# Optimization experiments

Measured on AMD Instinct MI355X. Metric: run time of the kernel, lower is better.

Reference implementation:

```python
import jax, jax.numpy as jnp
import numpy as np

EPS = 1e-5
K_NBR = 21   # num_neighbors + 1 (self)
PSI = 4


def _bn(x, g, b):
    # BatchNorm (training-mode forward): channel-last, normalize over all other axes
    axes = tuple(range(x.ndim - 1))
    m = jnp.mean(x, axis=axes, keepdims=True)
    v = jnp.var(x, axis=axes, keepdims=True)
    return (x - m) * jax.lax.rsqrt(v + EPS) * g + b


def setup_inputs() -> dict:
    key = jax.random.key(0)
    ks = jax.random.split(key, 16)
    B, N, Cin, Cout = 4, 2048, 64, 256
    h = Cout // 2
    w_ch = Cout // PSI
    heads = 2 * PSI - 1

    def w(k, o, i):
        return jax.random.normal(k, (o, i), dtype=jnp.float32) * (1.0 / np.sqrt(i))

    p = {}
    p['xyz'] = jax.random.normal(ks[0], (B, N, 3), dtype=jnp.float32)
    p['f'] = jax.random.normal(ks[1], (B, Cin, N), dtype=jnp.float32)
    p['W_geo'] = w(ks[2], h, 6);       p['g_geo'] = jnp.ones(h);   p['b_geo'] = jnp.zeros(h)
    p['W_feat'] = w(ks[3], h, 2 * Cin); p['g_feat'] = jnp.ones(h); p['b_feat'] = jnp.zeros(h)
    p['g_bn'] = jnp.ones(Cout); p['b_bn'] = jnp.zeros(Cout)
    p['W_q'] = w(ks[4], Cout, Cout); p['g_q'] = jnp.ones(Cout); p['b_q'] = jnp.zeros(Cout)
    p['W_k'] = w(ks[5], Cout, Cout); p['g_k'] = jnp.ones(Cout); p['b_k'] = jnp.zeros(Cout)
    p['W_v'] = w(ks[6], Cout, Cout); p['g_v'] = jnp.ones(Cout); p['b_v'] = jnp.zeros(Cout)
    p['W_fus'] = w(ks[7], Cout, heads * w_ch); p['bias_fus'] = jnp.zeros(Cout)
    p['g_fus'] = jnp.ones(Cout); p['b_fus'] = jnp.zeros(Cout)
    p['g_ln'] = jnp.ones(Cout); p['b_ln'] = jnp.zeros(Cout)
    p['W_mlp'] = w(ks[8], Cout, Cout); p['bias_mlp'] = jnp.zeros(Cout)
    return p


def reference(xyz, f, W_geo, g_geo, b_geo, W_feat, g_feat, b_feat, g_bn, b_bn,
              W_q, g_q, b_q, W_k, g_k, b_k, W_v, g_v, b_v,
              W_fus, bias_fus, g_fus, b_fus, g_ln, b_ln, W_mlp, bias_mlp):
    B, N, _ = xyz.shape
    Cout = g_bn.shape[0]
    w_ch = Cout // PSI
    d_sh = w_ch // 2
    heads = 2 * PSI - 1

    # ---- PositionFusion: KNN grouping ----
    sq = jnp.sum(xyz * xyz, axis=-1)                                   # [B,N]
    d2 = sq[:, :, None] + sq[:, None, :] - 2.0 * jnp.einsum('bnd,bmd->bnm', xyz, xyz)
    _, idx = jax.lax.top_k(-d2, K_NBR)                                 # [B,N,K]

    grouped_xyz = jax.vmap(lambda p, i: p[i])(xyz, idx)                # [B,N,K,3]
    xyz_diff = grouped_xyz - xyz[:, :, None, :]
    geo_in = jnp.concatenate(
        [jnp.broadcast_to(xyz[:, :, None, :], grouped_xyz.shape), xyz_diff], axis=-1)  # [B,N,K,6]

    ft = jnp.transpose(f, (0, 2, 1))                                   # [B,N,Cin]
    grouped_f = jax.vmap(lambda p, i: p[i])(ft, idx)                   # [B,N,K,Cin]
    feat_in = jnp.concatenate(
        [grouped_f, jnp.broadcast_to(ft[:, :, None, :], grouped_f.shape)], axis=-1)    # [B,N,K,2Cin]

    geo = jax.nn.relu(_bn(jnp.einsum('bnki,oi->bnko', geo_in, W_geo), g_geo, b_geo))
    fea = jax.nn.relu(_bn(jnp.einsum('bnki,oi->bnko', feat_in, W_feat), g_feat, b_feat))
    feature_ = jnp.max(jnp.concatenate([geo, fea], axis=-1), axis=2)   # [B,N,Cout] (maxpool over K)

    # ---- BatchNorm1d ----
    x = _bn(feature_, g_bn, b_bn)

    # ---- Shifted-channel multi-head attention ----
    q = jax.nn.relu(_bn(jnp.einsum('bnc,oc->bno', x, W_q), g_q, b_q))
    k = jax.nn.relu(_bn(jnp.einsum('bnc,oc->bno', x, W_k), g_k, b_k))
    v = jax.nn.relu(_bn(jnp.einsum('bnc,oc->bno', x, W_v), g_v, b_v))

    qh = jnp.stack([q[..., m * d_sh:m * d_sh + w_ch] for m in range(heads)], axis=1)  # [B,H,N,w]
    kh = jnp.stack([k[..., m * d_sh:m * d_sh + w_ch] for m in range(heads)], axis=1)
    vh = jnp.stack([v[..., m * d_sh:m * d_sh + w_ch] for m in range(heads)], axis=1)

    a = jax.nn.softmax(jnp.einsum('bhnc,bhmc->bhnm', qh, kh), axis=-1)  # [B,H,N,N]
    o = jnp.einsum('bhnm,bhmc->bhnc', a, vh)                            # [B,H,N,w]
    O = jnp.transpose(o, (0, 2, 1, 3)).reshape(B, N, heads * w_ch)      # channel-concat per head

    fus = jax.nn.relu(_bn(jnp.einsum('bnc,oc->bno', O, W_fus) + bias_fus, g_fus, b_fus))

    feature__ = fus + feature_                                          # residual

    # ---- LayerNorm over channels ----
    m = jnp.mean(feature__, axis=-1, keepdims=True)
    var = jnp.var(feature__, axis=-1, keepdims=True)
    y = (feature__ - m) * jax.lax.rsqrt(var + EPS) * g_ln + b_ln

    out = feature__ + (jnp.einsum('bnc,oc->bno', y, W_mlp) + bias_mlp)
    return jnp.transpose(out, (0, 2, 1))                                # [B,Cout,N] like torch
```

## Files before the change

### kernel.cpp

```cpp
#include <hip/hip_runtime.h>
#include <math.h>

#define NB    4
#define NPTS  2048
#define ROWS  (NB*NPTS)
#define CIN   64
#define COUT  256
#define KNBR  21
#define NHEADS 7
#define WCH   64
#define DSH   32
#define LOG2E 1.4426950408889634f

typedef __attribute__((ext_vector_type(8))) short short8;
typedef __attribute__((ext_vector_type(4))) float floatx4;

#if __has_builtin(__builtin_amdgcn_exp2f)
#define EXP2(x) __builtin_amdgcn_exp2f(x)
#else
#define EXP2(x) __expf((x)*0.6931471805599453f)
#endif
#if __has_builtin(__builtin_amdgcn_rcpf)
#define RCP(x) __builtin_amdgcn_rcpf(x)
#else
#define RCP(x) (1.0f/(x))
#endif

__device__ __forceinline__ ushort f2bf(float x) {
    unsigned u = __float_as_uint(x);
    u += 0x7fffu + ((u >> 16) & 1u);
    return (ushort)(u >> 16);
}

__device__ __forceinline__ unsigned cvt_pk_bf16(float lo, float hi) {
    unsigned r;
    asm("v_cvt_pk_bf16_f32 %0, %1, %2" : "=v"(r) : "v"(lo), "v"(hi));
    return r;
}

template<int CTRL, int RMASK>
__device__ __forceinline__ unsigned dpp_umin_step(unsigned x) {
    unsigned t = (unsigned)__builtin_amdgcn_update_dpp((int)x, (int)x, CTRL, RMASK, 0xF, false);
    return (t < x) ? t : x;
}
__device__ __forceinline__ unsigned wave_min_u32(unsigned x) {
    x = dpp_umin_step<0x111, 0xF>(x);
    x = dpp_umin_step<0x112, 0xF>(x);
    x = dpp_umin_step<0x114, 0xF>(x);
    x = dpp_umin_step<0x118, 0xF>(x);
    x = dpp_umin_step<0x142, 0xA>(x);
    x = dpp_umin_step<0x143, 0xC>(x);
    return (unsigned)__builtin_amdgcn_readlane((int)x, 63);
}

__global__ __launch_bounds__(256) void prep_knn(const float* __restrict__ f, const float* __restrict__ Wf,
                                                const float* __restrict__ xyz, const float* __restrict__ Wg,
                                                const float* __restrict__ W_q, const float* __restrict__ W_k,
                                                const float* __restrict__ W_v, const float* __restrict__ W_fus,
                                                float* __restrict__ X, float* __restrict__ A,
                                                ushort* __restrict__ Wb, float* __restrict__ sums,
                                                int* __restrict__ idx) {
    __shared__ float4 SXQ[2048];
    int t = threadIdx.x;
    int blk = blockIdx.x;
    if (blk < 512) {
        float* As = (float*)SXQ;
        float* Ws = As + 16*68;
        int bx = blk & 127, by = blk >> 7;
        if (by == 0 && bx < 12) sums[bx*256 + t] = 0.f;
        int gid = (by*128 + bx)*256 + t;
        for (int i = gid; i < 311296; i += 131072) {
            const float* Wsrc; int off;
            if (i < 65536)       { Wsrc = W_q;   off = i; }
            else if (i < 131072) { Wsrc = W_k;   off = i - 65536; }
            else if (i < 196608) { Wsrc = W_v;   off = i - 131072; }
            else                 { Wsrc = W_fus; off = i - 196608; }
            Wb[i] = f2bf(Wsrc[off]);
        }
        int r0 = bx * 64, n0 = by * 64;
        for (int e = t; e < 4096; e += 256) {
            int row = r0 + (e >> 6), c = n0 + (e & 63), cc = c & 127;
            float x = xyz[row*3], y = xyz[row*3+1], z = xyz[row*3+2];
            const float* w = Wg + cc*6;
            float s = (c < 128) ? ((w[3]*x + w[4]*y) + w[5]*z)
                                : (((w[0]-w[3])*x + (w[1]-w[4])*y) + (w[2]-w[5])*z);
            A[(size_t)row*256 + c] = s;
        }
        int b = r0 >> 11, nbase = r0 & 2047;
        int tx = t & 15, ty = t >> 4;
        float acc[4][4];
#pragma unroll
        for (int i = 0; i < 4; i++)
#pragma unroll
            for (int j = 0; j < 4; j++) acc[i][j] = 0.f;
        int m64 = t & 63, kg = t >> 6;
        int lk = t & 15, lm = t >> 4;
        for (int k0 = 0; k0 < 64; k0 += 16) {
#pragma unroll
            for (int p = 0; p < 4; p++) {
                int k = kg*4 + p;
                As[k*68 + m64] = f[(size_t)b*CIN*NPTS + (size_t)(k0 + k)*NPTS + nbase + m64];
            }
#pragma unroll
            for (int i2 = 0; i2 < 4; i2++) {
                int cg = n0 + lm + 16*i2;
                Ws[lk*68 + lm + 16*i2] = Wf[(size_t)(cg & 127)*128 + (cg >> 7)*64 + k0 + lk];
            }
            __syncthreads();
#pragma unroll
            for (int kq = 0; kq < 16; kq++) {
                float4 a  = *(const float4*)&As[kq*68 + 4*ty];
                float4 b4 = *(const float4*)&Ws[kq*68 + 4*tx];
                float av[4] = {a.x, a.y, a.z, a.w};
                float bv[4] = {b4.x, b4.y, b4.z, b4.w};
#pragma unroll
                for (int i = 0; i < 4; i++)
#pragma unroll
                    for (int j = 0; j < 4; j++) acc[i][j] = fmaf(av[i], bv[j], acc[i][j]);
            }
            __syncthreads();
        }
#pragma unroll
        for (int i = 0; i < 4; i++)
#pragma unroll
            for (int j = 0; j < 4; j++)
                X[(size_t)(r0 + 4*ty + i)*256 + n0 + 4*tx + j] = acc[i][j];
        return;
    }
    int kb = blk - 512;
    int b = kb >> 9;
    int g = kb & 511;
    for (int m = t; m < NPTS; m += 256) {
        float x = xyz[(size_t)b*NPTS*3 + m*3];
        float y = xyz[(size_t)b*NPTS*3 + m*3 + 1];
        float z = xyz[(size_t)b*NPTS*3 + m*3 + 2];
        SXQ[m] = make_float4(x, y, z, (x*x + y*y) + z*z);
    }
    __syncthreads();
    int w = t >> 6, lane = t & 63;
    int n = g*4 + w;
    float4 q4 = SXQ[n];
    float qx = q4.x, qy = q4.y, qz = q4.z, sqn = q4.w;
    unsigned key[32];
#pragma unroll
    for (int i = 0; i < 32; i++) {
        int m = lane + (i << 6);
        float4 p = SXQ[m];
        float dt = (qx*p.x + qy*p.y) + qz*p.z;
        float d2 = fmaxf((sqn + p.w) - 2.0f*dt, 0.f);
        key[i] = (__float_as_uint(d2) & 0xFFFFF800u) | (unsigned)m;
    }
    unsigned winkey = 0xFFFFFFFFu;
    for (int kk = 0; kk < 32; kk++) {
        unsigned lv = key[0];
#pragma unroll
        for (int i = 1; i < 32; i++) lv = (key[i] < lv) ? key[i] : lv;
        unsigned win = wave_min_u32(lv);
        if (lane == kk) winkey = win;
        unsigned widx = win & 2047u;
        int slot = (int)(widx >> 6);
        bool own = (lane == (int)(widx & 63u));
#pragma unroll
        for (int i = 0; i < 32; i++)
            if (i == slot && own) key[i] = 0xFFFFFFFFu;
    }
    double d2r;
    int mr;
    {
        double qx64 = (double)qx, qy64 = (double)qy, qz64 = (double)qz;
        double sqn64 = qx64*qx64 + qy64*qy64 + qz64*qz64;
        if (lane < 32) {
            mr = (int)(winkey & 2047u);
            float4 p = SXQ[mr];
            double x = (double)p.x, y = (double)p.y, z = (double)p.z;
            double sqm = x*x + y*y + z*z;
            double dt  = qx64*x + qy64*y + qz64*z;
            d2r = (sqn64 + sqm) - 2.0*dt;
        } else {
            d2r = INFINITY; mr = 0x7FFFFFFF;
        }
    }
#pragma unroll
    for (int k = 2; k <= 32; k <<= 1) {
#pragma unroll
        for (int j = k >> 1; j > 0; j >>= 1) {
            double od = __shfl_xor(d2r, j, 64);
            int    om = __shfl_xor(mr, j, 64);
            bool up    = ((lane & k) == 0);
            bool lower = ((lane & j) == 0);
            bool oless = (od < d2r) || (od == d2r && om < mr);
            bool keepOther = up ? (lower ? oless : !oless) : (lower ? !oless : oless);
            if (keepOther) { d2r = od; mr = om; }
        }
    }
    if (lane < KNBR)
        idx[((size_t)b*NPTS + n)*KNBR + lane] = mr;
}

__global__ __launch_bounds__(256) void stats_gf(const float* __restrict__ geoBC, const float* __restrict__ featAC,
                                                const int* __restrict__ idx, const float* __restrict__ g_geo,
                                                const float* __restrict__ g_feat,
                                                float* __restrict__ sums, float* __restrict__ xsel) {
    int c = threadIdx.x;
    int cc = c & 127;
    const float* base = (c < 128) ? geoBC : featAC;
    bool wantmax = ((c < 128) ? g_geo[cc] : g_feat[cc]) >= 0.f;
    float s = 0.f, ss = 0.f;
    int r0 = blockIdx.x * 32;
    for (int r = r0; r < r0 + 32; r++) {
        int b = r >> 11;
        float ctr = base[(size_t)r*256 + 128 + cc];
        float mx = -1e30f, mn = 1e30f;
        const int* ip = idx + (size_t)r*KNBR;
        for (int kk = 0; kk < KNBR; kk++) {
            int j = ip[kk];
            float xv = ctr + base[((size_t)(b*NPTS + j))*256 + cc];
            mx = fmaxf(mx, xv); mn = fminf(mn, xv);
            s += xv; ss += xv*xv;
        }
        xsel[(size_t)r*256 + c] = wantmax ? mx : mn;
    }
    atomicAdd(&sums[c], s);
    atomicAdd(&sums[256 + c], ss);
}

__global__ __launch_bounds__(256) void feature_maxsel(const float* __restrict__ xsel, const float* __restrict__ sums,
                                                      const float* __restrict__ g_geo, const float* __restrict__ b_geo,
                                                      const float* __restrict__ g_feat, const float* __restrict__ b_feat,
                                                      float* __restrict__ feat, float* __restrict__ sums_bn1) {
    int c = threadIdx.x;
    const float inv = 1.0f / (float)(ROWS*KNBR);
    float mean = sums[c]*inv;
    float var  = sums[256+c]*inv - mean*mean;
    float g  = (c < 128) ? g_geo[c] : g_feat[c-128];
    float bb = (c < 128) ? b_geo[c] : b_feat[c-128];
    float sc = g / sqrtf(var + 1e-5f);
    float tt = bb - mean*sc;
    float s = 0.f, ss = 0.f;
    int r0 = blockIdx.x*32;
    for (int r = r0; r < r0+32; r++) {
        size_t i = (size_t)r*256 + c;
        float y = fmaxf(fmaf(sc, xsel[i], tt), 0.f);
        feat[i] = y; s += y; ss += y*y;
    }
    atomicAdd(&sums_bn1[c], s); atomicAdd(&sums_bn1[256+c], ss);
}

__global__ __launch_bounds__(256) void gemm_qkv(const float* __restrict__ Af, const float* __restrict__ sums_in,
                                                const float* __restrict__ g_bn, const float* __restrict__ b_bn,
                                                const ushort* __restrict__ Wb,
                                                float* __restrict__ QKVF, float* __restrict__ sums) {
    __shared__ float bns[2][256];
    __shared__ float red[4][256][2];
    int t = threadIdx.x;
    int r0 = blockIdx.x * 64, g = blockIdx.y;
    int w = t >> 6, lane = t & 63;
    int r15 = lane & 15, quad = lane >> 4;
    {
        float mean = sums_in[512 + t] * (1.0f/(float)ROWS);
        float var  = sums_in[768 + t] * (1.0f/(float)ROWS) - mean*mean;
        float sc = g_bn[t] / sqrtf(var + 1e-5f);
        bns[0][t] = sc;
        bns[1][t] = b_bn[t] - mean*sc;
    }
    __syncthreads();
    short8 aq[8];
    {
        const float* ap = Af + (size_t)(r0 + 16*w + r15)*256;
#pragma unroll
        for (int kc = 0; kc < 8; kc++) {
            int k0 = 32*kc + 8*quad;
            float4 a0 = *(const float4*)&ap[k0];
            float4 a1 = *(const float4*)&ap[k0+4];
            float4 s0 = *(const float4*)&bns[0][k0];
            float4 s1 = *(const float4*)&bns[0][k0+4];
            float4 h0 = *(const float4*)&bns[1][k0];
            float4 h1 = *(const float4*)&bns[1][k0+4];
            ushort u8[8];
            u8[0] = f2bf(fmaf(s0.x, a0.x, h0.x)); u8[1] = f2bf(fmaf(s0.y, a0.y, h0.y));
            u8[2] = f2bf(fmaf(s0.z, a0.z, h0.z)); u8[3] = f2bf(fmaf(s0.w, a0.w, h0.w));
            u8[4] = f2bf(fmaf(s1.x, a1.x, h1.x)); u8[5] = f2bf(fmaf(s1.y, a1.y, h1.y));
            u8[6] = f2bf(fmaf(s1.z, a1.z, h1.z)); u8[7] = f2bf(fmaf(s1.w, a1.w, h1.w));
            aq[kc] = *(short8*)u8;
        }
    }
    floatx4 zero4 = {0.f, 0.f, 0.f, 0.f};
    floatx4 acc[16];
#pragma unroll
    for (int st = 0; st < 16; st++) acc[st] = zero4;
    const ushort* wbase = Wb + (size_t)g*65536 + (size_t)r15*256 + 8*quad;
#pragma unroll
    for (int st = 0; st < 16; st++) {
        const ushort* wp = wbase + (size_t)(16*st)*256;
#pragma unroll
        for (int kc = 0; kc < 8; kc++) {
            short8 bf = *(const short8*)(wp + 32*kc);
            acc[st] = __builtin_amdgcn_mfma_f32_16x16x32_bf16(aq[kc], bf, acc[st], 0, 0, 0);
        }
    }
#pragma unroll
    for (int st = 0; st < 16; st++) {
        float s  = (acc[st][0] + acc[st][1]) + (acc[st][2] + acc[st][3]);
        float q2 = (acc[st][0]*acc[st][0] + acc[st][1]*acc[st][1]) +
                   (acc[st][2]*acc[st][2] + acc[st][3]*acc[st][3]);
        s  += __shfl_xor(s, 16, 64);  s  += __shfl_xor(s, 32, 64);
        q2 += __shfl_xor(q2, 16, 64); q2 += __shfl_xor(q2, 32, 64);
        if (lane < 16) { red[w][16*st + r15][0] = s; red[w][16*st + r15][1] = q2; }
#pragma unroll
        for (int reg = 0; reg < 4; reg++)
            QKVF[(size_t)(r0 + 16*w + 4*quad + reg)*768 + g*256 + 16*st + r15] = acc[st][reg];
    }
    __syncthreads();
    {
        float s = red[0][t][0] + red[1][t][0] + red[2][t][0] + red[3][t][0];
        float q = red[0][t][1] + red[1][t][1] + red[2][t][1] + red[3][t][1];
        atomicAdd(&sums[1024 + g*512 + t], s);
        atomicAdd(&sums[1024 + g*512 + 256 + t], q);
    }
}

__global__ __launch_bounds__(256) void affine_qkv(const float* __restrict__ QKVF, const float* __restrict__ sums,
                                                  const float* __restrict__ g_q, const float* __restrict__ b_q,
                                                  const float* __restrict__ g_k, const float* __restrict__ b_k,
                                                  const float* __restrict__ g_v, const float* __restrict__ b_v,
                                                  ushort* __restrict__ qk, ushort* __restrict__ vt) {
    __shared__ float sts[6][256];
    __shared__ ushort tile[64][72];
    int t = threadIdx.x;
    {
        const float* gs[3] = {g_q, g_k, g_v};
        const float* bs[3] = {b_q, b_k, b_v};
#pragma unroll
        for (int g = 0; g < 3; g++) {
            float mean = sums[1024 + g*512 + t] * (1.0f/(float)ROWS);
            float var  = sums[1024 + g*512 + 256 + t] * (1.0f/(float)ROWS) - mean*mean;
            float sc = gs[g][t] / sqrtf(var + 1e-5f);
            float sh = bs[g][t] - mean*sc;
            if (g == 0) { sc *= LOG2E; sh *= LOG2E; }
            sts[2*g][t] = sc;
            sts[2*g+1][t] = sh;
        }
    }
    __syncthreads();
    int r0 = blockIdx.x * 64, c0 = blockIdx.y * 64;
    int b = r0 >> 11, nbase = r0 & 2047;
    if (c0 < 512) {
#pragma unroll
        for (int rep = 0; rep < 16; rep++) {
            int e = t + 256*rep;
            int row = e >> 6, c = e & 63;
            int col = c0 + c, g = col >> 8, cc = col & 255;
            float v = QKVF[(size_t)(r0 + row)*768 + col];
            v = fmaxf(fmaf(sts[2*g][cc], v, sts[2*g+1][cc]), 0.f);
            qk[(size_t)(r0 + row)*512 + col] = f2bf(v);
        }
    } else {
#pragma unroll
        for (int rep = 0; rep < 16; rep++) {
            int e = t + 256*rep;
            int row = e >> 6, c = e & 63;
            int col = c0 + c, cc = col & 255;
            float v = QKVF[(size_t)(r0 + row)*768 + col];
            v = fmaxf(fmaf(sts[4][cc], v, sts[5][cc]), 0.f);
            tile[c][row] = f2bf(v);
        }
        __syncthreads();
#pragma unroll
        for (int rep = 0; rep < 16; rep++) {
            int e = t + 256*rep;
            int cc = e >> 6, nn = e & 63;
            vt[((size_t)(b*256 + (c0 - 512) + cc))*2048 + nbase + nn] = tile[cc][nn];
        }
    }
}

__global__ __launch_bounds__(512) void attn2(const ushort* __restrict__ qk, const ushort* __restrict__ vt,
                                             float* __restrict__ obuf) {
    __shared__ ushort Ksh[64*72];
    __shared__ ushort Vts[64*72];
    __shared__ ushort Psh[128*72];
    int h = blockIdx.y, b = blockIdx.z;
    int r0 = blockIdx.x * 128;
    int t = threadIdx.x;
    int w = t >> 6, lane = t & 63;
    int r15 = lane & 15, quad = lane >> 4;
    size_t rowbase = (size_t)b*NPTS;
    int hoff = h*DSH;

    short8 aq[2];
#pragma unroll
    for (int s = 0; s < 2; s++)
        aq[s] = *(const short8*)(qk + (rowbase + r0 + 16*w + r15)*512 + hoff + 32*s + 8*quad);

    floatx4 zero4 = {0.f, 0.f, 0.f, 0.f};
    floatx4 oacc[4];
    float mrun = -1e30f, lrun = 0.f;
#pragma unroll
    for (int i = 0; i < 4; i++) oacc[i] = zero4;

    ushort* prow = &Psh[(16*w + r15)*72];

    for (int m0 = 0; m0 < NPTS; m0 += 64) {
        {
            int rr = t >> 3, c = t & 7;
            *(uint4*)&Ksh[rr*72 + 8*c] =
                *(const uint4*)(qk + (rowbase + m0 + rr)*512 + 256 + hoff + 8*c);
            *(uint4*)&Vts[rr*72 + 8*c] =
                *(const uint4*)(vt + ((size_t)(b*256 + hoff + rr))*2048 + m0 + 8*c);
        }
        __syncthreads();

        floatx4 sacc[4];
#pragma unroll
        for (int tt = 0; tt < 4; tt++) sacc[tt] = zero4;
#pragma unroll
        for (int tt = 0; tt < 4; tt++) {
            int key = 16*tt + r15;
#pragma unroll
            for (int s = 0; s < 2; s++) {
                short8 kf = *(const short8*)&Ksh[key*72 + 32*s + 8*quad];
                sacc[tt] = __builtin_amdgcn_mfma_f32_16x16x32_bf16(kf, aq[s], sacc[tt], 0, 0, 0);
            }
        }

        float mx = sacc[0][0];
#pragma unroll
        for (int tt = 0; tt < 4; tt++)
#pragma unroll
            for (int reg = 0; reg < 4; reg++) mx = fmaxf(mx, sacc[tt][reg]);
        mx = fmaxf(mx, __shfl_xor(mx, 16, 64));
        mx = fmaxf(mx, __shfl_xor(mx, 32, 64));

        if (!__all(mx <= mrun)) {
            float mnew = fmaxf(mrun, mx);
            float alpha = EXP2(mrun - mnew);
            lrun *= alpha;
#pragma unroll
            for (int td = 0; td < 4; td++) oacc[td] *= alpha;
            mrun = mnew;
        }

        float rs = 0.f;
#pragma unroll
        for (int tt = 0; tt < 4; tt++) {
            float p0 = EXP2(sacc[tt][0] - mrun);
            float p1 = EXP2(sacc[tt][1] - mrun);
            float p2 = EXP2(sacc[tt][2] - mrun);
            float p3 = EXP2(sacc[tt][3] - mrun);
            rs += (p0 + p1) + (p2 + p3);
            uint2 pk2;
            pk2.x = cvt_pk_bf16(p0, p1);
            pk2.y = cvt_pk_bf16(p2, p3);
            *(uint2*)&prow[16*tt + 4*quad] = pk2;
        }
        rs += __shfl_xor(rs, 16, 64);
        rs += __shfl_xor(rs, 32, 64);
        lrun += rs;

#pragma unroll
        for (int s = 0; s < 2; s++) {
            short8 pf = *(const short8*)&prow[32*s + 8*quad];
#pragma unroll
            for (int td = 0; td < 4; td++) {
                short8 vf = *(const short8*)&Vts[(16*td + r15)*72 + 32*s + 8*quad];
                oacc[td] = __builtin_amdgcn_mfma_f32_16x16x32_bf16(vf, pf, oacc[td], 0, 0, 0);
            }
        }
        __syncthreads();
    }

    float invl = RCP(lrun);
#pragma unroll
    for (int td = 0; td < 4; td++) {
        floatx4 o = oacc[td] * invl;
        *(float4*)&obuf[(rowbase + r0 + 16*w + r15)*(size_t)(NHEADS*WCH) + h*WCH + 16*td + 4*quad] =
            *(float4*)&o;
    }
}

__global__ __launch_bounds__(256) void gemm_fus(const float* __restrict__ OBUF, const ushort* __restrict__ Wb,
                                                const float* __restrict__ bias, float* __restrict__ C,
                                                float* __restrict__ sums) {
    __shared__ float red[4][128][2];
    int t = threadIdx.x;
    int r0 = blockIdx.x * 64, n0 = blockIdx.y * 128;
    int w = t >> 6, lane = t & 63;
    int r15 = lane & 15, quad = lane >> 4;
    int arow = 16*w + r15;
    short8 aq[14];
    {
        const float* p0 = OBUF + (size_t)(r0 + arow)*448;
#pragma unroll
        for (int kc = 0; kc < 14; kc++) {
            int k0 = 32*kc + 8*quad;
            float4 x0 = *(const float4*)&p0[k0];
            float4 y0 = *(const float4*)&p0[k0+4];
            ushort u8[8];
            u8[0] = f2bf(x0.x); u8[1] = f2bf(x0.y);
            u8[2] = f2bf(x0.z); u8[3] = f2bf(x0.w);
            u8[4] = f2bf(y0.x); u8[5] = f2bf(y0.y);
            u8[6] = f2bf(y0.z); u8[7] = f2bf(y0.w);
            aq[kc] = *(short8*)u8;
        }
    }
    floatx4 zero4 = {0.f, 0.f, 0.f, 0.f};
    floatx4 acc[8];
#pragma unroll
    for (int st = 0; st < 8; st++) acc[st] = zero4;
    const ushort* wbase = Wb + 196608 + (size_t)(n0 + r15)*448 + 8*quad;
#pragma unroll
    for (int st = 0; st < 8; st++) {
        const ushort* wp = wbase + (size_t)(16*st)*448;
#pragma unroll
        for (int kc = 0; kc < 14; kc++) {
            short8 bf = *(const short8*)(wp + 32*kc);
            acc[st] = __builtin_amdgcn_mfma_f32_16x16x32_bf16(aq[kc], bf, acc[st], 0, 0, 0);
        }
    }
#pragma unroll
    for (int st = 0; st < 8; st++) {
        int col = n0 + 16*st + r15;
        float bi = bias[col];
        float v0 = acc[st][0] + bi, v1 = acc[st][1] + bi, v2 = acc[st][2] + bi, v3 = acc[st][3] + bi;
        float s  = (v0 + v1) + (v2 + v3);
        float q2 = (v0*v0 + v1*v1) + (v2*v2 + v3*v3);
        s  += __shfl_xor(s, 16, 64);  s  += __shfl_xor(s, 32, 64);
        q2 += __shfl_xor(q2, 16, 64); q2 += __shfl_xor(q2, 32, 64);
        if (lane < 16) { red[w][16*st + r15][0] = s; red[w][16*st + r15][1] = q2; }
        C[(size_t)(r0 + 16*w + 4*quad + 0)*256 + col] = v0;
        C[(size_t)(r0 + 16*w + 4*quad + 1)*256 + col] = v1;
        C[(size_t)(r0 + 16*w + 4*quad + 2)*256 + col] = v2;
        C[(size_t)(r0 + 16*w + 4*quad + 3)*256 + col] = v3;
    }
    __syncthreads();
    {
        int col = t >> 1, which = t & 1;
        float v = red[0][col][which] + red[1][col][which] + red[2][col][which] + red[3][col][which];
        atomicAdd(&sums[2560 + which*256 + n0 + col], v);
    }
}

__global__ __launch_bounds__(256) void gemm_mlp_ln(const float* __restrict__ FUSP, const float* __restrict__ A,
                                                   const float* __restrict__ sums,
                                                   const float* __restrict__ g_fus, const float* __restrict__ b_fus,
                                                   const float* __restrict__ g_ln, const float* __restrict__ b_ln,
                                                   const float* __restrict__ W, const float* __restrict__ bias,
                                                   float* __restrict__ outp) {
    __shared__ float Ys[256][68];
    __shared__ float FFs[64][65];
    __shared__ float Ws[16][68];
    __shared__ float tr[64][65];
    __shared__ float SC[256], SH[256], GL[256], BL[256];
    int t = threadIdx.x;
    int r0 = blockIdx.x*64, n0 = blockIdx.y*64;
    {
        float mean0 = sums[2560 + t] * (1.0f/(float)ROWS);
        float var0  = sums[2560 + 256 + t] * (1.0f/(float)ROWS) - mean0*mean0;
        float sc = g_fus[t] / sqrtf(var0 + 1e-5f);
        SC[t] = sc; SH[t] = b_fus[t] - mean0*sc;
        GL[t] = g_ln[t]; BL[t] = b_ln[t];
    }
    __syncthreads();
    int row = t >> 2, seg = t & 3;
    size_t rb = (size_t)(r0 + row)*256;
    float4 vv[16];
    float s = 0.f, ss = 0.f;
#pragma unroll
    for (int j = 0; j < 16; j++) {
        int c = seg*64 + 4*j;
        float4 fp = *(const float4*)&FUSP[rb + c];
        float4 fe = *(const float4*)&A[rb + c];
        float4 sc4 = *(const float4*)&SC[c];
        float4 sh4 = *(const float4*)&SH[c];
        float4 v;
        v.x = fmaxf(fmaf(sc4.x, fp.x, sh4.x), 0.f) + fe.x;
        v.y = fmaxf(fmaf(sc4.y, fp.y, sh4.y), 0.f) + fe.y;
        v.z = fmaxf(fmaf(sc4.z, fp.z, sh4.z), 0.f) + fe.z;
        v.w = fmaxf(fmaf(sc4.w, fp.w, sh4.w), 0.f) + fe.w;
        vv[j] = v;
        s  += (v.x + v.y) + (v.z + v.w);
        ss += (v.x*v.x + v.y*v.y) + (v.z*v.z + v.w*v.w);
        if (seg == blockIdx.y) *(float4*)&FFs[row][4*j] = v;
    }
    s  += __shfl_xor(s, 1, 64);  s  += __shfl_xor(s, 2, 64);
    ss += __shfl_xor(ss, 1, 64); ss += __shfl_xor(ss, 2, 64);
    float mean = s * (1.f/256.f);
    float var  = ss * (1.f/256.f) - mean*mean;
    float rin  = 1.f/sqrtf(var + 1e-5f);
#pragma unroll
    for (int j = 0; j < 16; j++) {
        int c = seg*64 + 4*j;
        float4 gl = *(const float4*)&GL[c];
        float4 bl = *(const float4*)&BL[c];
        float4 v = vv[j];
        Ys[c+0][row] = (v.x - mean)*rin*gl.x + bl.x;
        Ys[c+1][row] = (v.y - mean)*rin*gl.y + bl.y;
        Ys[c+2][row] = (v.z - mean)*rin*gl.z + bl.z;
        Ys[c+3][row] = (v.w - mean)*rin*gl.w + bl.w;
    }
    __syncthreads();
    int tx = t & 15, ty = t >> 4;
    int lk = t & 15, lm = t >> 4;
    float acc[4][4];
#pragma unroll
    for (int i = 0; i < 4; i++)
#pragma unroll
        for (int j = 0; j < 4; j++) acc[i][j] = 0.f;
    for (int k0 = 0; k0 < 256; k0 += 16) {
#pragma unroll
        for (int i2 = 0; i2 < 4; i2++)
            Ws[lk][lm + 16*i2] = W[(size_t)(n0 + lm + 16*i2)*256 + k0 + lk];
        __syncthreads();
#pragma unroll
        for (int kq = 0; kq < 16; kq++) {
            float4 a  = *(const float4*)&Ys[k0 + kq][4*ty];
            float4 b4 = *(const float4*)&Ws[kq][4*tx];
            float av[4] = {a.x, a.y, a.z, a.w};
            float bv[4] = {b4.x, b4.y, b4.z, b4.w};
#pragma unroll
            for (int i = 0; i < 4; i++)
#pragma unroll
                for (int j = 0; j < 4; j++) acc[i][j] = fmaf(av[i], bv[j], acc[i][j]);
        }
        __syncthreads();
    }
#pragma unroll
    for (int i = 0; i < 4; i++)
#pragma unroll
        for (int j = 0; j < 4; j++) {
            float v = acc[i][j] + bias[n0 + 4*tx + j] + FFs[4*ty + i][4*tx + j];
            tr[4*tx + j][4*ty + i] = v;
        }
    __syncthreads();
    int b = r0 >> 11, nbase = r0 & 2047;
#pragma unroll
    for (int rep = 0; rep < 16; rep++) {
        int e = t + 256*rep;
        int cl = e >> 6, nl = e & 63;
        outp[((size_t)(b*256 + n0 + cl))*2048 + nbase + nl] = tr[cl][nl];
    }
}

extern "C" void kernel_launch(void* const* d_in, const int* in_sizes, int n_in,
                              void* d_out, int out_size, void* d_ws, size_t ws_size,
                              hipStream_t stream) {
    const float* xyz    = (const float*)d_in[0];
    const float* f      = (const float*)d_in[1];
    const float* W_geo  = (const float*)d_in[2];
    const float* g_geo  = (const float*)d_in[3];
    const float* b_geo  = (const float*)d_in[4];
    const float* W_feat = (const float*)d_in[5];
    const float* g_feat = (const float*)d_in[6];
    const float* b_feat = (const float*)d_in[7];
    const float* g_bn   = (const float*)d_in[8];
    const float* b_bn   = (const float*)d_in[9];
    const float* W_q    = (const float*)d_in[10];
    const float* g_q    = (const float*)d_in[11];
    const float* b_q    = (const float*)d_in[12];
    const float* W_k    = (const float*)d_in[13];
    const float* g_k    = (const float*)d_in[14];
    const float* b_k    = (const float*)d_in[15];
    const float* W_v    = (const float*)d_in[16];
    const float* g_v    = (const float*)d_in[17];
    const float* b_v    = (const float*)d_in[18];
    const float* W_fus  = (const float*)d_in[19];
    const float* bias_fus = (const float*)d_in[20];
    const float* g_fus  = (const float*)d_in[21];
    const float* b_fus  = (const float*)d_in[22];
    const float* g_ln   = (const float*)d_in[23];
    const float* b_ln   = (const float*)d_in[24];
    const float* W_mlp  = (const float*)d_in[25];
    const float* bias_mlp = (const float*)d_in[26];

    float* ws = (float*)d_ws;
    const size_t MBF = 262144;
    float* SUMS  = ws;
    int*   IDX   = (int*)(ws + 16384);
    float* A     = ws + 1*MBF;
    float* X     = ws + 9*MBF;
    ushort* QK16 = (ushort*)(ws + 9*MBF);
    float* FUSP  = ws + 9*MBF;
    float* CSEL  = ws + 17*MBF;
    float* QKVF  = ws + 17*MBF;
    float* OBUF  = ws + 17*MBF;
    ushort* VT16 = (ushort*)(ws + 45*MBF);
    ushort* WB16 = (ushort*)(ws + 49*MBF);

    prep_knn<<<2560, 256, 0, stream>>>(f, W_feat, xyz, W_geo, W_q, W_k, W_v, W_fus,
                                       X, A, WB16, SUMS, IDX);
    stats_gf<<<256, 256, 0, stream>>>(A, X, IDX, g_geo, g_feat, SUMS, CSEL);
    feature_maxsel<<<256, 256, 0, stream>>>(CSEL, SUMS, g_geo, b_geo, g_feat, b_feat, A, SUMS + 512);
    gemm_qkv<<<dim3(128, 3), 256, 0, stream>>>(A, SUMS, g_bn, b_bn, WB16, QKVF, SUMS);
    affine_qkv<<<dim3(128, 12), 256, 0, stream>>>(QKVF, SUMS, g_q, b_q, g_k, b_k, g_v, b_v, QK16, VT16);
    attn2<<<dim3(NPTS/128, NHEADS, NB), 512, 0, stream>>>(QK16, VT16, OBUF);
    gemm_fus<<<dim3(128, 2), 256, 0, stream>>>(OBUF, WB16, bias_fus, FUSP, SUMS);
    gemm_mlp_ln<<<dim3(128, 4), 256, 0, stream>>>(FUSP, A, SUMS, g_fus, b_fus, g_ln, b_ln,
                                                  W_mlp, bias_mlp, (float*)d_out);
}
```

Baseline: 396.0 us.

## Double-buffer K/V tiles in attention with register prefetch and priority hints

The attention kernel now keeps two LDS buffers for K and V. The next tile's global loads are issued into registers at the top of each iteration, so they overlap with the QK and PV MFMA work, and are written to the alternate buffer afterwards, leaving one barrier per iteration. s_setprio hints are placed around the MFMA sections. The cost is twice the LDS for K/V, extra VGPRs for the prefetched data, and one redundant wrapped load on the final iteration.

```diff
diff --git a/kernel.cpp b/kernel.cpp
--- a/kernel.cpp
+++ b/kernel.cpp
@@ -376,8 +376,8 @@
 
 __global__ __launch_bounds__(512) void attn2(const ushort* __restrict__ qk, const ushort* __restrict__ vt,
                                              float* __restrict__ obuf) {
-    __shared__ ushort Ksh[64*72];
-    __shared__ ushort Vts[64*72];
+    __shared__ ushort Ksh[2][64*72];
+    __shared__ ushort Vts[2][64*72];
     __shared__ ushort Psh[128*72];
     int h = blockIdx.y, b = blockIdx.z;
     int r0 = blockIdx.x * 128;
@@ -386,11 +386,23 @@
     int r15 = lane & 15, quad = lane >> 4;
     size_t rowbase = (size_t)b*NPTS;
     int hoff = h*DSH;
+    int rr = t >> 3, c8 = t & 7;
+
+    const ushort* ksrc = qk + (rowbase + rr)*512 + 256 + hoff + 8*c8;
+    const ushort* vsrc = vt + ((size_t)(b*256 + hoff + rr))*2048 + 8*c8;
+    int ldst = rr*72 + 8*c8;
 
     short8 aq[2];
 #pragma unroll
     for (int s = 0; s < 2; s++)
         aq[s] = *(const short8*)(qk + (rowbase + r0 + 16*w + r15)*512 + hoff + 32*s + 8*quad);
+
+    {
+        uint4 k0 = *(const uint4*)(ksrc);
+        uint4 v0 = *(const uint4*)(vsrc);
+        *(uint4*)&Ksh[0][ldst] = k0;
+        *(uint4*)&Vts[0][ldst] = v0;
+    }
 
     floatx4 zero4 = {0.f, 0.f, 0.f, 0.f};
     floatx4 oacc[4];
@@ -400,28 +412,33 @@
 
     ushort* prow = &Psh[(16*w + r15)*72];
 
+    asm volatile("s_waitcnt lgkmcnt(0)" ::: "memory");
+    __builtin_amdgcn_s_barrier();
+    __builtin_amdgcn_sched_barrier(0);
+
+    int cur = 0;
     for (int m0 = 0; m0 < NPTS; m0 += 64) {
-        {
-            int rr = t >> 3, c = t & 7;
-            *(uint4*)&Ksh[rr*72 + 8*c] =
-                *(const uint4*)(qk + (rowbase + m0 + rr)*512 + 256 + hoff + 8*c);
-            *(uint4*)&Vts[rr*72 + 8*c] =
-                *(const uint4*)(vt + ((size_t)(b*256 + hoff + rr))*2048 + m0 + 8*c);
-        }
-        __syncthreads();
+        int mnext = (m0 + 64 < NPTS) ? (m0 + 64) : 0;
+        uint4 kreg = *(const uint4*)(ksrc + (size_t)mnext*512);
+        uint4 vreg = *(const uint4*)(vsrc + mnext);
+
+        const ushort* Kc = Ksh[cur];
+        const ushort* Vc = Vts[cur];
 
         floatx4 sacc[4];
 #pragma unroll
         for (int tt = 0; tt < 4; tt++) sacc[tt] = zero4;
+        __builtin_amdgcn_s_setprio(1);
 #pragma unroll
         for (int tt = 0; tt < 4; tt++) {
             int key = 16*tt + r15;
 #pragma unroll
             for (int s = 0; s < 2; s++) {
-                short8 kf = *(const short8*)&Ksh[key*72 + 32*s + 8*quad];
+                short8 kf = *(const short8*)&Kc[key*72 + 32*s + 8*quad];
                 sacc[tt] = __builtin_amdgcn_mfma_f32_16x16x32_bf16(kf, aq[s], sacc[tt], 0, 0, 0);
             }
         }
+        __builtin_amdgcn_s_setprio(0);
 
         float mx = sacc[0][0];
 #pragma unroll
@@ -457,16 +474,26 @@
         rs += __shfl_xor(rs, 32, 64);
         lrun += rs;
 
+        __builtin_amdgcn_s_setprio(1);
 #pragma unroll
         for (int s = 0; s < 2; s++) {
             short8 pf = *(const short8*)&prow[32*s + 8*quad];
 #pragma unroll
             for (int td = 0; td < 4; td++) {
-                short8 vf = *(const short8*)&Vts[(16*td + r15)*72 + 32*s + 8*quad];
+                short8 vf = *(const short8*)&Vts[cur][(16*td + r15)*72 + 32*s + 8*quad];
                 oacc[td] = __builtin_amdgcn_mfma_f32_16x16x32_bf16(vf, pf, oacc[td], 0, 0, 0);
             }
         }
-        __syncthreads();
+        __builtin_amdgcn_s_setprio(0);
+        (void)Vc;
+
+        *(uint4*)&Ksh[cur ^ 1][ldst] = kreg;
+        *(uint4*)&Vts[cur ^ 1][ldst] = vreg;
+        cur ^= 1;
+
+        asm volatile("s_waitcnt lgkmcnt(0)" ::: "memory");
+        __builtin_amdgcn_s_barrier();
+        __builtin_amdgcn_sched_barrier(0);
     }
 
     float invl = RCP(lrun);
```

Result: no change. 392.6 us (-0.9%).
